# Kernel optimization log

Measured on AMD Instinct MI355X. Metric: run time of the kernel, lower is better.

## Reference

```python
import jax, jax.numpy as jnp
import numpy as np

B, NQ, NK, E, H, F, L = 8, 300, 4096, 256, 8, 2048, 6
D = E // H
SCALE = D ** -0.5


def _ln(x, g, b):
    m = x.mean(-1, keepdims=True)
    v = ((x - m) ** 2).mean(-1, keepdims=True)
    return (x - m) / jnp.sqrt(v + 1e-5) * g + b


def _split_heads(x):
    b, n, _ = x.shape
    return x.reshape(b, n, H, D).transpose(0, 2, 1, 3)  # (B,H,N,D)


def _merge_heads(x):
    b, h, n, d = x.shape
    return x.transpose(0, 2, 1, 3).reshape(b, n, h * d)


def setup_inputs() -> dict:
    key = jax.random.key(0)
    c = [0]
    def nk():
        c[0] += 1
        return jax.random.fold_in(key, c[0])
    def p(shape):
        return jax.random.normal(nk(), shape, jnp.float32) * 0.02
    return {
        "tgt": jax.random.normal(nk(), (B, NQ, E), jnp.float32),
        "memory": jax.random.normal(nk(), (B, NK, E), jnp.float32),
        "geometry_mask": jax.random.randint(nk(), (B, NQ, NK), 0, 2).astype(bool),
        "sa_wqkv": p((L, 3 * E, E)), "sa_bqkv": p((L, 3 * E)),
        "sa_wo": p((L, E, E)), "sa_bo": p((L, E)),
        "ca_wq": p((L, E, E)), "ca_bq": p((L, E)),
        "ca_wk": p((L, E, E)), "ca_bk": p((L, E)),
        "ca_wv": p((L, E, E)), "ca_bv": p((L, E)),
        "ca_wo": p((L, E, E)), "ca_bo": p((L, E)),
        "f_w1": p((L, F, E)), "f_b1": p((L, F)),
        "f_w2": p((L, E, F)), "f_b2": p((L, E)),
        "ln1g": jnp.ones((L, E)), "ln1b": jnp.zeros((L, E)),
        "ln2g": jnp.ones((L, E)), "ln2b": jnp.zeros((L, E)),
        "ln3g": jnp.ones((L, E)), "ln3b": jnp.zeros((L, E)),
        "lnfg": jnp.ones((E,)), "lnfb": jnp.zeros((E,)),
    }


def _forward(tgt, memory, geometry_mask, params):
    mask4 = geometry_mask[:, None, :, :]  # (B,1,NQ,NK), broadcast over heads

    def step(t, p):
        (wqkv, bqkv, wo, bo, wq, bq, wk, bk, wv, bv, wco, bco,
         w1, b1, w2, b2, g1, be1, g2, be2, g3, be3) = p
        # --- self-attention (torch nn.MultiheadAttention, eval mode) ---
        qkv = t @ wqkv.T + bqkv
        q, k, v = jnp.split(qkv, 3, axis=-1)
        q, k, v = _split_heads(q), _split_heads(k), _split_heads(v)
        a = jax.nn.softmax(jnp.einsum('bhqd,bhkd->bhqk', q, k) * SCALE, axis=-1)
        sa = _merge_heads(jnp.einsum('bhqk,bhkd->bhqd', a, v)) @ wo.T + bo
        t = _ln(t + sa, g1, be1)
        # --- geometry-constrained cross-attention ---
        q = _split_heads(t @ wq.T + bq)
        k = _split_heads(memory @ wk.T + bk)
        v = _split_heads(memory @ wv.T + bv)
        s = jnp.einsum('bhqd,bhkd->bhqk', q, k) * SCALE
        s = jnp.where(mask4, s, -jnp.inf)  # masked_fill(~mask, -inf)
        a = jax.nn.softmax(s, axis=-1)
        ca = _merge_heads(jnp.einsum('bhqk,bhkd->bhqd', a, v)) @ wco.T + bco
        t = _ln(t + ca, g2, be2)
        # --- FFN ---
        f = jax.nn.relu(t @ w1.T + b1) @ w2.T + b2
        t = _ln(t + f, g3, be3)
        return t, None

    out, _ = jax.lax.scan(step, tgt, params)
    return out


def reference(tgt, memory, geometry_mask, sa_wqkv, sa_bqkv, sa_wo, sa_bo,
              ca_wq, ca_bq, ca_wk, ca_bk, ca_wv, ca_bv, ca_wo, ca_bo,
              f_w1, f_b1, f_w2, f_b2, ln1g, ln1b, ln2g, ln2b, ln3g, ln3b,
              lnfg, lnfb):
    params = (sa_wqkv, sa_bqkv, sa_wo, sa_bo, ca_wq, ca_bq, ca_wk, ca_bk,
              ca_wv, ca_bv, ca_wo, ca_bo, f_w1, f_b1, f_w2, f_b2,
              ln1g, ln1b, ln2g, ln2b, ln3g, ln3b)
    out = _forward(tgt, memory, geometry_mask, params)
    return _ln(out, lnfg, lnfb)
```

## Files before the change

### kernel.cpp

```cpp
#include <hip/hip_runtime.h>
#include <hip/hip_bf16.h>

constexpr int cB = 8, cNQ = 300, cNK = 4096, cE = 256, cH = 8, cD = 32, cF = 2048, cL = 6;
constexpr int MT = cB * cNQ;
constexpr int MM = cB * cNK;
constexpr int cQT = 10;
constexpr int cKS = 4;
constexpr float kScale = 0.17677669529663687f;

typedef __attribute__((ext_vector_type(8))) short short8_t;
typedef __attribute__((ext_vector_type(4))) short short4_t;
typedef __attribute__((ext_vector_type(4))) float float4_t;

__device__ inline short f2bf(float x) {
  __hip_bfloat16 h = __float2bfloat16(x);
  return __builtin_bit_cast(short, h);
}

__global__ void init_t(const float* __restrict__ in, float* __restrict__ t,
                       __hip_bfloat16* __restrict__ tb, int n) {
  int i = blockIdx.x * 256 + threadIdx.x;
  if (i < n) { float v = in[i]; t[i] = v; tb[i] = __float2bfloat16(v); }
}
__global__ void cast_f32_bf16(const float* __restrict__ in, __hip_bfloat16* __restrict__ out, int n) {
  int i = blockIdx.x * 256 + threadIdx.x;
  if (i < n) out[i] = __float2bfloat16(in[i]);
}

__global__ void pack_mask_T(const int* __restrict__ m, unsigned* __restrict__ mT) {
  int key = blockIdx.x * 256 + threadIdx.x;
  int qt = blockIdx.y, b = blockIdx.z;
  unsigned w = 0;
  for (int j = 0; j < 32; ++j) {
    int q = qt * 32 + j;
    unsigned bit = (q < cNQ) ? (unsigned)(m[((size_t)b * cNQ + q) * cNK + key] != 0) : 0u;
    w |= bit << j;
  }
  mT[((size_t)b * cQT + qt) * cNK + key] = w;
}

template<typename TA, typename TW, int EPI, int OMODE, typename TOUT>
__global__ __launch_bounds__(256) void gemm_mfma(const TA* __restrict__ A,
                                                 const TW* __restrict__ W,
                                                 const float* __restrict__ bias,
                                                 TOUT* __restrict__ C,
                                                 int M, int N, int K) {
  constexpr int LDSS = 72;
  __shared__ short As[64][LDSS];
  __shared__ short Ws[64][LDSS];
  int tid = threadIdx.x;
  int bm = blockIdx.x * 64, bn = blockIdx.y * 64;
  int lane = tid & 63, wave = tid >> 6;
  int m16 = lane & 15, quad = lane >> 4;
  int wm = (wave >> 1) * 32, wn = (wave & 1) * 32;

  int srow = tid >> 2;
  int kc = (tid & 3) * 16;
  bool aok = (bm + srow) < M;

  float4_t acc[2][2];
#pragma unroll
  for (int i = 0; i < 2; ++i)
#pragma unroll
    for (int j = 0; j < 2; ++j) acc[i][j] = (float4_t){0.f, 0.f, 0.f, 0.f};

  for (int k0 = 0; k0 < K; k0 += 64) {
    if constexpr (__hip_internal::is_same<TA, float>::value) {
      const float* src = A + (size_t)(bm + srow) * K + k0 + kc;
      short8_t p0, p1;
#pragma unroll
      for (int u = 0; u < 8; ++u) p0[u] = aok ? f2bf(src[u]) : (short)0;
#pragma unroll
      for (int u = 0; u < 8; ++u) p1[u] = aok ? f2bf(src[8 + u]) : (short)0;
      *(short8_t*)&As[srow][kc] = p0;
      *(short8_t*)&As[srow][kc + 8] = p1;
    } else {
      const TA* src = A + (size_t)(bm + srow) * K + k0 + kc;
      short8_t z = 0;
      *(short8_t*)&As[srow][kc] = aok ? *(const short8_t*)src : z;
      *(short8_t*)&As[srow][kc + 8] = aok ? *(const short8_t*)(src + 8) : z;
    }
    if constexpr (__hip_internal::is_same<TW, float>::value) {
      const float* src = W + (size_t)(bn + srow) * K + k0 + kc;
      short8_t p0, p1;
#pragma unroll
      for (int u = 0; u < 8; ++u) p0[u] = f2bf(src[u]);
#pragma unroll
      for (int u = 0; u < 8; ++u) p1[u] = f2bf(src[8 + u]);
      *(short8_t*)&Ws[srow][kc] = p0;
      *(short8_t*)&Ws[srow][kc + 8] = p1;
    } else {
      const TW* src = W + (size_t)(bn + srow) * K + k0 + kc;
      *(short8_t*)&Ws[srow][kc] = *(const short8_t*)src;
      *(short8_t*)&Ws[srow][kc + 8] = *(const short8_t*)(src + 8);
    }
    __syncthreads();
#pragma unroll
    for (int kk = 0; kk < 2; ++kk) {
      short8_t aF[2], bF[2];
#pragma unroll
      for (int i = 0; i < 2; ++i)
        aF[i] = *(const short8_t*)&As[wm + i * 16 + m16][kk * 32 + quad * 8];
#pragma unroll
      for (int j = 0; j < 2; ++j)
        bF[j] = *(const short8_t*)&Ws[wn + j * 16 + m16][kk * 32 + quad * 8];
#pragma unroll
      for (int i = 0; i < 2; ++i)
#pragma unroll
        for (int j = 0; j < 2; ++j)
          acc[i][j] = __builtin_amdgcn_mfma_f32_16x16x32_bf16(aF[i], bF[j], acc[i][j], 0, 0, 0);
    }
    __syncthreads();
  }

  if constexpr (OMODE == 2) {
#pragma unroll
    for (int i = 0; i < 2; ++i)
#pragma unroll
      for (int r = 0; r < 4; ++r) {
        int ml = wm + i * 16 + quad * 4 + r;
#pragma unroll
        for (int j = 0; j < 2; ++j) {
          int nl = wn + j * 16 + m16;
          Ws[nl][ml] = f2bf(acc[i][j][r] + bias[bn + nl]);
        }
      }
    __syncthreads();
    int nl = tid >> 2, mc = (tid & 3) * 16;
    if (bm + mc < M) {
      int n = bn + nl;
      __hip_bfloat16* dst = (__hip_bfloat16*)C +
          ((size_t)(n >> 5) * 32 + (n & 31)) * (size_t)M + bm + mc;
      *(short8_t*)dst = *(const short8_t*)&Ws[nl][mc];
      *(short8_t*)(dst + 8) = *(const short8_t*)&Ws[nl][mc + 8];
    }
  } else {
#pragma unroll
    for (int i = 0; i < 2; ++i) {
#pragma unroll
      for (int r = 0; r < 4; ++r) {
        int m = bm + wm + i * 16 + quad * 4 + r;
        if (m >= M) continue;
#pragma unroll
        for (int j = 0; j < 2; ++j) {
          int n = bn + wn + j * 16 + m16;
          float v = acc[i][j][r] + bias[n];
          if (EPI == 1) v = fmaxf(v, 0.f);
          if constexpr (OMODE == 1) {
            ((__hip_bfloat16*)C)[((size_t)(n >> 5) * M + m) * 32 + (n & 31)] = __float2bfloat16(v);
          } else if constexpr (__hip_internal::is_same<TOUT, float>::value) {
            C[(size_t)m * N + n] = v;
          } else {
            C[(size_t)m * N + n] = __float2bfloat16(v);
          }
        }
      }
    }
  }
}

template<typename TW, int EPI, int OMODE, typename TOUT>
__global__ __launch_bounds__(256) void gemm128(const __hip_bfloat16* __restrict__ A,
                                               const TW* __restrict__ W,
                                               const float* __restrict__ bias,
                                               TOUT* __restrict__ C,
                                               int M, int N, int K) {
  __shared__ short lds[2 * 128 * 72];
  auto As = (short(*)[72])lds;
  auto Ws = (short(*)[72])(lds + 128 * 72);
  int tid = threadIdx.x;
  int bm = blockIdx.x * 128, bn = blockIdx.y * 128;
  int lane = tid & 63, wave = tid >> 6;
  int n16 = lane & 15, quad = lane >> 4;
  int wm = (wave >> 1) * 64, wn = (wave & 1) * 64;
  int srow = tid >> 1, kc = (tid & 1) * 32;
  bool aok = (bm + srow) < M;

  float4_t acc[4][4];
#pragma unroll
  for (int i = 0; i < 4; ++i)
#pragma unroll
    for (int j = 0; j < 4; ++j) acc[i][j] = (float4_t){0.f, 0.f, 0.f, 0.f};

  for (int k0 = 0; k0 < K; k0 += 64) {
    {
      const __hip_bfloat16* src = A + (size_t)(bm + srow) * K + k0 + kc;
      short8_t z = 0;
#pragma unroll
      for (int u = 0; u < 4; ++u)
        *(short8_t*)&As[srow][kc + u * 8] = aok ? *(const short8_t*)(src + u * 8) : z;
    }
    if constexpr (__hip_internal::is_same<TW, float>::value) {
      const float* src = W + (size_t)(bn + srow) * K + k0 + kc;
#pragma unroll
      for (int u = 0; u < 4; ++u) {
        short8_t p;
#pragma unroll
        for (int v = 0; v < 8; ++v) p[v] = f2bf(src[u * 8 + v]);
        *(short8_t*)&Ws[srow][kc + u * 8] = p;
      }
    } else {
      const TW* src = W + (size_t)(bn + srow) * K + k0 + kc;
#pragma unroll
      for (int u = 0; u < 4; ++u)
        *(short8_t*)&Ws[srow][kc + u * 8] = *(const short8_t*)(src + u * 8);
    }
    __syncthreads();
#pragma unroll
    for (int kk = 0; kk < 2; ++kk) {
      short8_t aF[4], bF[4];
#pragma unroll
      for (int i = 0; i < 4; ++i)
        aF[i] = *(const short8_t*)&As[wm + i * 16 + n16][kk * 32 + quad * 8];
#pragma unroll
      for (int j = 0; j < 4; ++j)
        bF[j] = *(const short8_t*)&Ws[wn + j * 16 + n16][kk * 32 + quad * 8];
#pragma unroll
      for (int i = 0; i < 4; ++i)
#pragma unroll
        for (int j = 0; j < 4; ++j)
          acc[i][j] = __builtin_amdgcn_mfma_f32_16x16x32_bf16(aF[i], bF[j], acc[i][j], 0, 0, 0);
    }
    __syncthreads();
  }

  if constexpr (OMODE == 2) {
    auto TT = (short(*)[128])lds;
#pragma unroll
    for (int i = 0; i < 4; ++i)
#pragma unroll
      for (int r = 0; r < 4; ++r) {
        int ml = wm + i * 16 + quad * 4 + r;
#pragma unroll
        for (int j = 0; j < 4; ++j) {
          int nl = wn + j * 16 + n16;
          TT[nl][ml] = f2bf(acc[i][j][r] + bias[bn + nl]);
        }
      }
    __syncthreads();
    int nl = tid >> 1, mh = (tid & 1) * 64;
    int n = bn + nl;
    __hip_bfloat16* dst = (__hip_bfloat16*)C +
        ((size_t)(n >> 5) * 32 + (n & 31)) * (size_t)M + bm + mh;
#pragma unroll
    for (int ch = 0; ch < 8; ++ch) {
      if (bm + mh + ch * 8 < M)
        *(short8_t*)(dst + ch * 8) = *(const short8_t*)&TT[nl][mh + ch * 8];
    }
  } else {
#pragma unroll
    for (int i = 0; i < 4; ++i) {
#pragma unroll
      for (int r = 0; r < 4; ++r) {
        int m = bm + wm + i * 16 + quad * 4 + r;
        if (m >= M) continue;
#pragma unroll
        for (int j = 0; j < 4; ++j) {
          int n = bn + wn + j * 16 + n16;
          float v = acc[i][j][r] + bias[n];
          if (EPI == 1) v = fmaxf(v, 0.f);
          if constexpr (OMODE == 1) {
            ((__hip_bfloat16*)C)[((size_t)(n >> 5) * M + m) * 32 + (n & 31)] = __float2bfloat16(v);
          } else if constexpr (__hip_internal::is_same<TOUT, float>::value) {
            C[(size_t)m * N + n] = v;
          } else {
            C[(size_t)m * N + n] = __float2bfloat16(v);
          }
        }
      }
    }
  }
}

template<typename TQ, bool MASKED>
__global__ __launch_bounds__(256) void attn_flash(
    const TQ* __restrict__ qb, size_t strQb, size_t strQh, int qRowStr,
    const __hip_bfloat16* __restrict__ kb, size_t strKb, size_t strKh, int kRowStr,
    const __hip_bfloat16* __restrict__ vt, size_t strVb, size_t strVh, size_t strVd,
    const unsigned* __restrict__ mT, size_t strMb,
    float* __restrict__ pO, size_t pStrO,
    float* __restrict__ pL, size_t pStrL,
    int nq, int nk, int kChunk) {
  int hb = blockIdx.x;
  int h = hb & 7, bz = hb >> 3;
  int qt = blockIdx.y, ks = blockIdx.z;
  int qbase = qt * 32;

  const TQ* q = qb + (size_t)bz * strQb + (size_t)h * strQh;
  const __hip_bfloat16* K = kb + (size_t)bz * strKb + (size_t)h * strKh;
  const __hip_bfloat16* V = vt + (size_t)bz * strVb + (size_t)h * strVh;
  const unsigned* mrow = MASKED ? (mT + (size_t)bz * strMb + (size_t)qt * cNK) : nullptr;

  int tid = threadIdx.x;
  int lane = tid & 63, wave = tid >> 6;
  int n16 = lane & 15, quad = lane >> 4;

  __shared__ float redO[4][32][33];
  __shared__ float redL[4][32];
  short* sPw = (short*)&redO[0][0][0] + wave * (32 * 40);

  short8_t qf[2];
#pragma unroll
  for (int qi = 0; qi < 2; ++qi) {
    qf[qi] = 0;
    int qr = qbase + qi * 16 + n16;
    if (qr < nq) {
      const TQ* qp = q + (size_t)qr * qRowStr + quad * 8;
      if constexpr (__hip_internal::is_same<TQ, float>::value) {
#pragma unroll
        for (int j = 0; j < 8; ++j) qf[qi][j] = f2bf(qp[j]);
      } else {
        qf[qi] = *(const short8_t*)qp;
      }
    }
  }
  short8_t ones;
#pragma unroll
  for (int j = 0; j < 8; ++j) ones[j] = f2bf(1.0f);

  float4_t accO[2][2], accL[2];
#pragma unroll
  for (int qi = 0; qi < 2; ++qi) {
    accL[qi] = (float4_t){0.f, 0.f, 0.f, 0.f};
#pragma unroll
    for (int di = 0; di < 2; ++di) accO[qi][di] = (float4_t){0.f, 0.f, 0.f, 0.f};
  }
  float4_t zero4 = {0.f, 0.f, 0.f, 0.f};

  int kpad = (nk + 31) & ~31;
  int kend = ks * kChunk + kChunk;
  if (kend > kpad) kend = kpad;
  for (int koff = ks * kChunk + wave * 32; koff < kend; koff += 128) {
    int k0 = koff + 2 * n16;
    unsigned w0 = 0xFFFFFFFFu, w1 = 0xFFFFFFFFu;
    if (MASKED) {
      const unsigned* mp = mrow + k0;
      w0 = mp[0]; w1 = mp[1];
    }
    bool in0 = k0 < nk, in1 = (k0 + 1) < nk;
    short8_t kf0 = *(const short8_t*)(K + (size_t)k0 * kRowStr + quad * 8);
    short8_t kf1 = *(const short8_t*)(K + (size_t)(k0 + 1) * kRowStr + quad * 8);
    short8_t vf0 = *(const short8_t*)(V + (size_t)n16 * strVd + koff + quad * 8);
    short8_t vf1 = *(const short8_t*)(V + (size_t)(16 + n16) * strVd + koff + quad * 8);
    __builtin_amdgcn_s_setprio(1);
    float4_t s00 = __builtin_amdgcn_mfma_f32_16x16x32_bf16(qf[0], kf0, zero4, 0, 0, 0);
    float4_t s01 = __builtin_amdgcn_mfma_f32_16x16x32_bf16(qf[0], kf1, zero4, 0, 0, 0);
    float4_t s10 = __builtin_amdgcn_mfma_f32_16x16x32_bf16(qf[1], kf0, zero4, 0, 0, 0);
    float4_t s11 = __builtin_amdgcn_mfma_f32_16x16x32_bf16(qf[1], kf1, zero4, 0, 0, 0);
    __builtin_amdgcn_s_setprio(0);
#pragma unroll
    for (int qi = 0; qi < 2; ++qi) {
      const float4_t& sa = qi ? s10 : s00;
      const float4_t& sb = qi ? s11 : s01;
#pragma unroll
      for (int r = 0; r < 4; ++r) {
        int row = qi * 16 + quad * 4 + r;
        bool ok0 = in0, ok1 = in1;
        if (MASKED) {
          ok0 = ok0 && ((w0 >> row) & 1u);
          ok1 = ok1 && ((w1 >> row) & 1u);
        }
        float p0 = ok0 ? __expf(sa[r] * kScale) : 0.f;
        float p1 = ok1 ? __expf(sb[r] * kScale) : 0.f;
        unsigned pw = (unsigned)(unsigned short)f2bf(p0) |
                      ((unsigned)(unsigned short)f2bf(p1) << 16);
        *(unsigned*)&sPw[row * 40 + 2 * n16] = pw;
      }
    }
    __builtin_amdgcn_s_setprio(1);
#pragma unroll
    for (int qi = 0; qi < 2; ++qi) {
      short8_t pf = *(const short8_t*)&sPw[(qi * 16 + n16) * 40 + quad * 8];
      accO[qi][0] = __builtin_amdgcn_mfma_f32_16x16x32_bf16(pf, vf0, accO[qi][0], 0, 0, 0);
      accO[qi][1] = __builtin_amdgcn_mfma_f32_16x16x32_bf16(pf, vf1, accO[qi][1], 0, 0, 0);
      accL[qi]    = __builtin_amdgcn_mfma_f32_16x16x32_bf16(pf, ones, accL[qi], 0, 0, 0);
    }
    __builtin_amdgcn_s_setprio(0);
  }

  __syncthreads();
#pragma unroll
  for (int qi = 0; qi < 2; ++qi) {
#pragma unroll
    for (int r = 0; r < 4; ++r) {
      int row = qi * 16 + quad * 4 + r;
#pragma unroll
      for (int di = 0; di < 2; ++di)
        redO[wave][row][di * 16 + n16] = accO[qi][di][r];
      if (n16 == 0) redL[wave][row] = accL[qi][r];
    }
  }
  __syncthreads();

  size_t oBase = (size_t)ks * pStrO + (size_t)(bz * cNQ) * 256 + h * 32;
  int row = tid >> 3, c0 = (tid & 7) * 4;
  if (qbase + row < nq) {
    float4_t o;
#pragma unroll
    for (int u = 0; u < 4; ++u)
      o[u] = redO[0][row][c0 + u] + redO[1][row][c0 + u] +
             redO[2][row][c0 + u] + redO[3][row][c0 + u];
    *(float4_t*)&pO[oBase + (size_t)(qbase + row) * 256 + c0] = o;
  }
  if (tid < 32 && qbase + tid < nq) {
    float l = redL[0][tid] + redL[1][tid] + redL[2][tid] + redL[3][tid];
    pL[(size_t)ks * pStrL + (size_t)hb * 320 + qbase + tid] = l;
  }
}

__global__ __launch_bounds__(64) void attn_merge(const float* __restrict__ pO,
                                                 const float* __restrict__ pL,
                                                 __hip_bfloat16* __restrict__ out) {
  int row = blockIdx.x;
  int lane = threadIdx.x;
  int c0 = lane * 4;
  int bz = row / cNQ, qq = row - bz * cNQ;
  int h = c0 >> 5;
  float l = 0.f;
#pragma unroll
  for (int ks = 0; ks < cKS; ++ks)
    l += pL[(size_t)ks * (64 * 320) + (size_t)(bz * 8 + h) * 320 + qq];
  float inv = 1.f / l;
  float o[4] = {0.f, 0.f, 0.f, 0.f};
#pragma unroll
  for (int ks = 0; ks < cKS; ++ks) {
    const float4_t v = *(const float4_t*)&pO[(size_t)ks * (MT * 256) + (size_t)row * 256 + c0];
#pragma unroll
    for (int u = 0; u < 4; ++u) o[u] += v[u];
  }
  short4_t res = {f2bf(o[0] * inv), f2bf(o[1] * inv), f2bf(o[2] * inv), f2bf(o[3] * inv)};
  *(short4_t*)&out[(size_t)row * 256 + c0] = res;
}

__global__ __launch_bounds__(64) void add_ln_k(float* __restrict__ t,
                                               __hip_bfloat16* __restrict__ tb,
                                               const float* __restrict__ delta,
                                               const float* __restrict__ g,
                                               const float* __restrict__ bb) {
  int r = blockIdx.x, lane = threadIdx.x;
  size_t base = (size_t)r * cE + lane * 4;
  float x[4];
  float s = 0.f;
#pragma unroll
  for (int i = 0; i < 4; ++i) { x[i] = t[base + i] + delta[base + i]; s += x[i]; }
  for (int off = 32; off; off >>= 1) s += __shfl_xor(s, off);
  float mean = s * (1.f / cE);
  float v = 0.f;
#pragma unroll
  for (int i = 0; i < 4; ++i) { float dd = x[i] - mean; v += dd * dd; }
  for (int off = 32; off; off >>= 1) v += __shfl_xor(v, off);
  float rstd = rsqrtf(v * (1.f / cE) + 1e-5f);
  float y[4];
#pragma unroll
  for (int i = 0; i < 4; ++i) {
    y[i] = (x[i] - mean) * rstd * g[lane * 4 + i] + bb[lane * 4 + i];
    t[base + i] = y[i];
  }
  short4_t pb = {f2bf(y[0]), f2bf(y[1]), f2bf(y[2]), f2bf(y[3])};
  *(short4_t*)&tb[base] = pb;
}

__global__ __launch_bounds__(64) void final_ln_k(const float* __restrict__ t,
                                                 const float* __restrict__ g,
                                                 const float* __restrict__ bb,
                                                 float* __restrict__ out) {
  int r = blockIdx.x, lane = threadIdx.x;
  size_t base = (size_t)r * cE + lane * 4;
  float x[4];
  float s = 0.f;
#pragma unroll
  for (int i = 0; i < 4; ++i) { x[i] = t[base + i]; s += x[i]; }
  for (int off = 32; off; off >>= 1) s += __shfl_xor(s, off);
  float mean = s * (1.f / cE);
  float v = 0.f;
#pragma unroll
  for (int i = 0; i < 4; ++i) { float dd = x[i] - mean; v += dd * dd; }
  for (int off = 32; off; off >>= 1) v += __shfl_xor(v, off);
  float rstd = rsqrtf(v * (1.f / cE) + 1e-5f);
#pragma unroll
  for (int i = 0; i < 4; ++i)
    out[base + i] = (x[i] - mean) * rstd * g[lane * 4 + i] + bb[lane * 4 + i];
}

struct Bufs {
  float *t, *s1, *s2, *pO, *pL;
  __hip_bfloat16 *tb, *big2, *vtq, *s1b, *s2b, *qbf, *ffnh, *kbuf, *vtb, *membf;
  unsigned* mTr;
  const float* memory;
  bool fullKV, precast;
};

template<typename TW>
static void run_layers(const TW* const* wt, const float* const* bs,
                       const float* ln1g, const float* ln1b,
                       const float* ln2g, const float* ln2b,
                       const float* ln3g, const float* ln3b,
                       Bufs B, hipStream_t stream) {
  const size_t pStrO = (size_t)MT * 256, pStrL = 64 * 320;
  for (int l = 0; l < cL; ++l) {
    const TW* wqkv = wt[0] + (size_t)l * 3 * cE * cE;  const float* bqkv = bs[0] + (size_t)l * 3 * cE;
    const TW* wo   = wt[1] + (size_t)l * cE * cE;      const float* bo   = bs[1] + (size_t)l * cE;
    const TW* wq   = wt[2] + (size_t)l * cE * cE;      const float* bq   = bs[2] + (size_t)l * cE;
    const TW* wk   = wt[3] + (size_t)l * cE * cE;      const float* bk   = bs[3] + (size_t)l * cE;
    const TW* wv   = wt[4] + (size_t)l * cE * cE;      const float* bv   = bs[4] + (size_t)l * cE;
    const TW* wco  = wt[5] + (size_t)l * cE * cE;      const float* bco  = bs[5] + (size_t)l * cE;
    const TW* w1   = wt[6] + (size_t)l * cF * cE;      const float* b1   = bs[6] + (size_t)l * cF;
    const TW* w2   = wt[7] + (size_t)l * cE * cF;      const float* b2   = bs[7] + (size_t)l * cE;

    gemm_mfma<__hip_bfloat16, TW, 0, 0, __hip_bfloat16><<<dim3(38, 8), 256, 0, stream>>>(
        B.tb, wqkv, bqkv, B.big2, MT, 512, cE);
    gemm_mfma<__hip_bfloat16, TW, 0, 2, __hip_bfloat16><<<dim3(38, 4), 256, 0, stream>>>(
        B.tb, wqkv + (size_t)512 * cE, bqkv + 512, B.vtq, MT, cE, cE);
    attn_flash<__hip_bfloat16, false><<<dim3(64, cQT, cKS), 256, 0, stream>>>(
        B.big2, (size_t)cNQ * 512, 32, 512,
        B.big2 + 256, (size_t)cNQ * 512, 32, 512,
        B.vtq, 300, (size_t)cD * MT, MT,
        nullptr, 0,
        B.pO, pStrO, B.pL, pStrL, cNQ, cNQ, 96);
    attn_merge<<<MT, 64, 0, stream>>>(B.pO, B.pL, B.s1b);
    gemm_mfma<__hip_bfloat16, TW, 0, 0, float><<<dim3(38, 4), 256, 0, stream>>>(
        B.s1b, wo, bo, B.s2, MT, cE, cE);
    add_ln_k<<<MT, 64, 0, stream>>>(B.t, B.tb, B.s2, ln1g + (size_t)l * cE, ln1b + (size_t)l * cE);
    gemm_mfma<__hip_bfloat16, TW, 0, 0, __hip_bfloat16><<<dim3(38, 4), 256, 0, stream>>>(
        B.tb, wq, bq, B.qbf, MT, cE, cE);
    if (B.fullKV && B.precast) {
      gemm128<TW, 0, 1, __hip_bfloat16><<<dim3(256, 2), 256, 0, stream>>>(
          B.membf, wk, bk, B.kbuf, MM, cE, cE);
      gemm128<TW, 0, 2, __hip_bfloat16><<<dim3(256, 2), 256, 0, stream>>>(
          B.membf, wv, bv, B.vtb, MM, cE, cE);
      attn_flash<__hip_bfloat16, true><<<dim3(64, cQT, cKS), 256, 0, stream>>>(
          B.qbf, (size_t)cNQ * cE, 32, cE,
          B.kbuf, (size_t)cNK * cD, (size_t)MM * cD, cD,
          B.vtb, (size_t)cNK, (size_t)cD * MM, MM,
          B.mTr, (size_t)cQT * cNK,
          B.pO, pStrO, B.pL, pStrL, cNQ, cNK, 1024);
      attn_merge<<<MT, 64, 0, stream>>>(B.pO, B.pL, B.s2b);
    } else {
      for (int b = 0; b < cB; ++b) {
        const float* memb = B.memory + (size_t)b * cNK * cE;
        gemm_mfma<float, TW, 0, 1, __hip_bfloat16><<<dim3(64, 4), 256, 0, stream>>>(
            memb, wk, bk, B.kbuf, cNK, cE, cE);
        gemm_mfma<float, TW, 0, 2, __hip_bfloat16><<<dim3(64, 4), 256, 0, stream>>>(
            memb, wv, bv, B.vtb, cNK, cE, cE);
        attn_flash<__hip_bfloat16, true><<<dim3(8, cQT, cKS), 256, 0, stream>>>(
            B.qbf + (size_t)b * cNQ * cE, 0, 32, cE,
            B.kbuf, 0, (size_t)cNK * cD, cD,
            B.vtb, 0, (size_t)cD * cNK, cNK,
            B.mTr + (size_t)b * cQT * cNK, 0,
            B.pO + (size_t)b * cNQ * 256, pStrO, B.pL + (size_t)b * 8 * 320, pStrL,
            cNQ, cNK, 1024);
      }
      attn_merge<<<MT, 64, 0, stream>>>(B.pO, B.pL, B.s2b);
    }
    gemm_mfma<__hip_bfloat16, TW, 0, 0, float><<<dim3(38, 4), 256, 0, stream>>>(
        B.s2b, wco, bco, B.s1, MT, cE, cE);
    add_ln_k<<<MT, 64, 0, stream>>>(B.t, B.tb, B.s1, ln2g + (size_t)l * cE, ln2b + (size_t)l * cE);
    gemm128<TW, 1, 0, __hip_bfloat16><<<dim3(19, 16), 256, 0, stream>>>(
        B.tb, w1, b1, B.ffnh, MT, cF, cE);
    gemm_mfma<__hip_bfloat16, TW, 0, 0, float><<<dim3(38, 4), 256, 0, stream>>>(
        B.ffnh, w2, b2, B.s1, MT, cE, cF);
    add_ln_k<<<MT, 64, 0, stream>>>(B.t, B.tb, B.s1, ln3g + (size_t)l * cE, ln3b + (size_t)l * cE);
  }
}

extern "C" void kernel_launch(void* const* d_in, const int* in_sizes, int n_in,
                              void* d_out, int out_size, void* d_ws, size_t ws_size,
                              hipStream_t stream) {
  (void)in_sizes; (void)n_in; (void)out_size;
  const float* tgt    = (const float*)d_in[0];
  const float* memory = (const float*)d_in[1];
  const int*   gmask  = (const int*)d_in[2];
  const float* w_in[8]  = {(const float*)d_in[3], (const float*)d_in[5], (const float*)d_in[7],
                           (const float*)d_in[9], (const float*)d_in[11], (const float*)d_in[13],
                           (const float*)d_in[15], (const float*)d_in[17]};
  const float* b_in[8]  = {(const float*)d_in[4], (const float*)d_in[6], (const float*)d_in[8],
                           (const float*)d_in[10], (const float*)d_in[12], (const float*)d_in[14],
                           (const float*)d_in[16], (const float*)d_in[18]};
  const size_t w_sz[8]  = {(size_t)cL*3*cE*cE, (size_t)cL*cE*cE, (size_t)cL*cE*cE,
                           (size_t)cL*cE*cE, (size_t)cL*cE*cE, (size_t)cL*cE*cE,
                           (size_t)cL*cF*cE, (size_t)cL*cE*cF};
  const float* ln1g = (const float*)d_in[19], *ln1b = (const float*)d_in[20];
  const float* ln2g = (const float*)d_in[21], *ln2b = (const float*)d_in[22];
  const float* ln3g = (const float*)d_in[23], *ln3b = (const float*)d_in[24];
  const float* lnfg = (const float*)d_in[25], *lnfb = (const float*)d_in[26];

  char* wp = (char*)d_ws;
  auto alloc = [&](size_t bytes) { void* p = wp; wp += (bytes + 255) & ~(size_t)255; return p; };

  Bufs B;
  B.memory = memory;
  B.t  = (float*)alloc((size_t)MT * cE * 4);
  B.s1 = (float*)alloc((size_t)MT * cE * 4);
  B.s2 = (float*)alloc((size_t)MT * cE * 4);
  B.tb = (__hip_bfloat16*)alloc((size_t)MT * cE * 2);
  B.big2 = (__hip_bfloat16*)alloc((size_t)MT * 512 * 2);
  B.vtq  = (__hip_bfloat16*)alloc((size_t)cH * cD * MT * 2);
  B.mTr = (unsigned*)alloc((size_t)cB * cQT * cNK * 4);
  B.pO = (float*)alloc((size_t)cKS * MT * 256 * 4);
  B.pL = (float*)alloc((size_t)cKS * 64 * 320 * 4);
  B.s1b = B.big2;
  B.s2b = B.big2 + (size_t)MT * 256;
  B.qbf = (__hip_bfloat16*)B.s1;
  B.ffnh = (__hip_bfloat16*)B.pO;

  size_t kvFull = (size_t)cH * MM * cD * 2;
  size_t used = (size_t)(wp - (char*)d_ws);
  B.fullKV = ws_size >= used + 2 * kvFull;
  if (B.fullKV) {
    B.kbuf = (__hip_bfloat16*)alloc(kvFull);
    B.vtb  = (__hip_bfloat16*)alloc(kvFull);
  } else {
    B.kbuf = (__hip_bfloat16*)alloc((size_t)cH * cNK * cD * 2);
    B.vtb  = (__hip_bfloat16*)alloc((size_t)cH * cNK * cD * 2);
  }
  size_t memBytes = (size_t)MM * cE * 2;
  used = (size_t)(wp - (char*)d_ws);
  B.precast = B.fullKV && (ws_size >= used + memBytes);
  B.membf = B.precast ? (__hip_bfloat16*)alloc(memBytes) : nullptr;

  size_t wbfTotal = 0;
  for (int i = 0; i < 8; ++i) wbfTotal += ((w_sz[i] * 2 + 255) & ~(size_t)255);
  used = (size_t)(wp - (char*)d_ws);
  bool wPre = ws_size >= used + wbfTotal;
  __hip_bfloat16* wbf[8] = {};
  if (wPre)
    for (int i = 0; i < 8; ++i) wbf[i] = (__hip_bfloat16*)alloc(w_sz[i] * 2);

  init_t<<<(MT * cE + 255) / 256, 256, 0, stream>>>(tgt, B.t, B.tb, MT * cE);
  pack_mask_T<<<dim3(cNK / 256, cQT, cB), 256, 0, stream>>>(gmask, B.mTr);
  if (B.precast)
    cast_f32_bf16<<<(MM * cE + 255) / 256, 256, 0, stream>>>(memory, B.membf, MM * cE);
  if (wPre)
    for (int i = 0; i < 8; ++i)
      cast_f32_bf16<<<(int)((w_sz[i] + 255) / 256), 256, 0, stream>>>(w_in[i], wbf[i], (int)w_sz[i]);

  if (wPre) {
    const __hip_bfloat16* wt[8];
    for (int i = 0; i < 8; ++i) wt[i] = wbf[i];
    run_layers<__hip_bfloat16>(wt, b_in, ln1g, ln1b, ln2g, ln2b, ln3g, ln3b, B, stream);
  } else {
    run_layers<float>(w_in, b_in, ln1g, ln1b, ln2g, ln2b, ln3g, ln3b, B, stream);
  }

  final_ln_k<<<MT, 64, 0, stream>>>(B.t, lnfg, lnfb, (float*)d_out);
}
```

Baseline: 1.282 ms.

## Add small-tile gemm32 for E-wide GEMMs and fold softmax scale into Q projection

Adds a 32x64-tile MFMA GEMM kernel and uses it for the four N=256 projections (out-proj, cross Q, cross out, FFN down). The smaller tiles launch 300 blocks instead of 152, so more CUs have work. The Q projections are pre-scaled by scale*log2(e), which lets the attention kernels use exp2f directly. Masking now multiplies by a float 0/1 instead of branching, and bf16 packing uses a paired conversion. The small-tile GEMM trades parallelism for less data reuse and no double buffering, notably on the K=2048 FFN GEMM.

```diff
diff --git a/kernel.cpp b/kernel.cpp
--- a/kernel.cpp
+++ b/kernel.cpp
@@ -7,6 +7,7 @@
 constexpr int cQT = 10;
 constexpr int cKS = 4;
 constexpr float kScale = 0.17677669529663687f;
+constexpr float kC2 = 0.25506601f;
 
 typedef __attribute__((ext_vector_type(8))) short short8_t;
 typedef __attribute__((ext_vector_type(4))) short short4_t;
@@ -15,6 +16,13 @@
 __device__ inline short f2bf(float x) {
   __hip_bfloat16 h = __float2bfloat16(x);
   return __builtin_bit_cast(short, h);
+}
+
+__device__ inline unsigned pack_bf16x2(float a, float b) {
+  __hip_bfloat162 pp = __float22bfloat162_rn(make_float2(a, b));
+  unsigned r;
+  __builtin_memcpy(&r, &pp, 4);
+  return r;
 }
 
 __global__ void init_t(const float* __restrict__ in, float* __restrict__ t,
@@ -146,6 +154,8 @@
           int n = bn + wn + j * 16 + m16;
           float v = acc[i][j][r] + bias[n];
           if (EPI == 1) v = fmaxf(v, 0.f);
+          if (EPI == 2 && n < 256) v *= kC2;
+          if (EPI == 3) v *= kC2;
           if constexpr (OMODE == 1) {
             ((__hip_bfloat16*)C)[((size_t)(n >> 5) * M + m) * 32 + (n & 31)] = __float2bfloat16(v);
           } else if constexpr (__hip_internal::is_same<TOUT, float>::value) {
@@ -154,6 +164,82 @@
             C[(size_t)m * N + n] = __float2bfloat16(v);
           }
         }
+      }
+    }
+  }
+}
+
+template<typename TW, int EPI, typename TOUT>
+__global__ __launch_bounds__(256) void gemm32(const __hip_bfloat16* __restrict__ A,
+                                              const TW* __restrict__ W,
+                                              const float* __restrict__ bias,
+                                              TOUT* __restrict__ C,
+                                              int M, int N, int K) {
+  __shared__ short As[32][72];
+  __shared__ short Ws[64][72];
+  int tid = threadIdx.x;
+  int bm = blockIdx.x * 32, bn = blockIdx.y * 64;
+  int lane = tid & 63, wave = tid >> 6;
+  int m16 = lane & 15, quad = lane >> 4;
+  int wn = wave * 16;
+
+  int sa_row = tid >> 3, sa_c = (tid & 7) * 8;
+  int sw_row = tid >> 2, sw_c = (tid & 3) * 16;
+  bool aok = (bm + sa_row) < M;
+
+  float4_t acc[2];
+  acc[0] = (float4_t){0.f, 0.f, 0.f, 0.f};
+  acc[1] = (float4_t){0.f, 0.f, 0.f, 0.f};
+
+  for (int k0 = 0; k0 < K; k0 += 64) {
+    {
+      const __hip_bfloat16* src = A + (size_t)(bm + sa_row) * K + k0 + sa_c;
+      short8_t z = 0;
+      *(short8_t*)&As[sa_row][sa_c] = aok ? *(const short8_t*)src : z;
+    }
+    if constexpr (__hip_internal::is_same<TW, float>::value) {
+      const float* src = W + (size_t)(bn + sw_row) * K + k0 + sw_c;
+      short8_t p0, p1;
+#pragma unroll
+      for (int u = 0; u < 8; ++u) p0[u] = f2bf(src[u]);
+#pragma unroll
+      for (int u = 0; u < 8; ++u) p1[u] = f2bf(src[8 + u]);
+      *(short8_t*)&Ws[sw_row][sw_c] = p0;
+      *(short8_t*)&Ws[sw_row][sw_c + 8] = p1;
+    } else {
+      const TW* src = W + (size_t)(bn + sw_row) * K + k0 + sw_c;
+      *(short8_t*)&Ws[sw_row][sw_c] = *(const short8_t*)src;
+      *(short8_t*)&Ws[sw_row][sw_c + 8] = *(const short8_t*)(src + 8);
+    }
+    __syncthreads();
+#pragma unroll
+    for (int kk = 0; kk < 2; ++kk) {
+      short8_t aF[2], bF;
+#pragma unroll
+      for (int i = 0; i < 2; ++i)
+        aF[i] = *(const short8_t*)&As[i * 16 + m16][kk * 32 + quad * 8];
+      bF = *(const short8_t*)&Ws[wn + m16][kk * 32 + quad * 8];
+#pragma unroll
+      for (int i = 0; i < 2; ++i)
+        acc[i] = __builtin_amdgcn_mfma_f32_16x16x32_bf16(aF[i], bF, acc[i], 0, 0, 0);
+    }
+    __syncthreads();
+  }
+
+#pragma unroll
+  for (int i = 0; i < 2; ++i) {
+#pragma unroll
+    for (int r = 0; r < 4; ++r) {
+      int m = bm + i * 16 + quad * 4 + r;
+      if (m >= M) continue;
+      int n = bn + wn + m16;
+      float v = acc[i][r] + bias[n];
+      if (EPI == 1) v = fmaxf(v, 0.f);
+      if (EPI == 3) v *= kC2;
+      if constexpr (__hip_internal::is_same<TOUT, float>::value) {
+        C[(size_t)m * N + n] = v;
+      } else {
+        C[(size_t)m * N + n] = __float2bfloat16(v);
       }
     }
   }
@@ -332,12 +418,15 @@
   if (kend > kpad) kend = kpad;
   for (int koff = ks * kChunk + wave * 32; koff < kend; koff += 128) {
     int k0 = koff + 2 * n16;
-    unsigned w0 = 0xFFFFFFFFu, w1 = 0xFFFFFFFFu;
+    unsigned w0 = 0, w1 = 0;
+    float okf0 = 1.f, okf1 = 1.f;
     if (MASKED) {
-      const unsigned* mp = mrow + k0;
-      w0 = mp[0]; w1 = mp[1];
-    }
-    bool in0 = k0 < nk, in1 = (k0 + 1) < nk;
+      uint2 mw = *(const uint2*)(mrow + k0);
+      w0 = mw.x; w1 = mw.y;
+    } else {
+      okf0 = (k0 < nk) ? 1.f : 0.f;
+      okf1 = (k0 + 1 < nk) ? 1.f : 0.f;
+    }
     short8_t kf0 = *(const short8_t*)(K + (size_t)k0 * kRowStr + quad * 8);
     short8_t kf1 = *(const short8_t*)(K + (size_t)(k0 + 1) * kRowStr + quad * 8);
     short8_t vf0 = *(const short8_t*)(V + (size_t)n16 * strVd + koff + quad * 8);
@@ -355,16 +444,16 @@
 #pragma unroll
       for (int r = 0; r < 4; ++r) {
         int row = qi * 16 + quad * 4 + r;
-        bool ok0 = in0, ok1 = in1;
+        float m0, m1;
         if (MASKED) {
-          ok0 = ok0 && ((w0 >> row) & 1u);
-          ok1 = ok1 && ((w1 >> row) & 1u);
+          m0 = (float)((w0 >> row) & 1u);
+          m1 = (float)((w1 >> row) & 1u);
+        } else {
+          m0 = okf0; m1 = okf1;
         }
-        float p0 = ok0 ? __expf(sa[r] * kScale) : 0.f;
-        float p1 = ok1 ? __expf(sb[r] * kScale) : 0.f;
-        unsigned pw = (unsigned)(unsigned short)f2bf(p0) |
-                      ((unsigned)(unsigned short)f2bf(p1) << 16);
-        *(unsigned*)&sPw[row * 40 + 2 * n16] = pw;
+        float p0 = exp2f(sa[r]) * m0;
+        float p1 = exp2f(sb[r]) * m1;
+        *(unsigned*)&sPw[row * 40 + 2 * n16] = pack_bf16x2(p0, p1);
       }
     }
     __builtin_amdgcn_s_setprio(1);
@@ -507,7 +596,7 @@
     const TW* w1   = wt[6] + (size_t)l * cF * cE;      const float* b1   = bs[6] + (size_t)l * cF;
     const TW* w2   = wt[7] + (size_t)l * cE * cF;      const float* b2   = bs[7] + (size_t)l * cE;
 
-    gemm_mfma<__hip_bfloat16, TW, 0, 0, __hip_bfloat16><<<dim3(38, 8), 256, 0, stream>>>(
+    gemm_mfma<__hip_bfloat16, TW, 2, 0, __hip_bfloat16><<<dim3(38, 8), 256, 0, stream>>>(
         B.tb, wqkv, bqkv, B.big2, MT, 512, cE);
     gemm_mfma<__hip_bfloat16, TW, 0, 2, __hip_bfloat16><<<dim3(38, 4), 256, 0, stream>>>(
         B.tb, wqkv + (size_t)512 * cE, bqkv + 512, B.vtq, MT, cE, cE);
@@ -518,10 +607,10 @@
         nullptr, 0,
         B.pO, pStrO, B.pL, pStrL, cNQ, cNQ, 96);
     attn_merge<<<MT, 64, 0, stream>>>(B.pO, B.pL, B.s1b);
-    gemm_mfma<__hip_bfloat16, TW, 0, 0, float><<<dim3(38, 4), 256, 0, stream>>>(
+    gemm32<TW, 0, float><<<dim3(75, 4), 256, 0, stream>>>(
         B.s1b, wo, bo, B.s2, MT, cE, cE);
     add_ln_k<<<MT, 64, 0, stream>>>(B.t, B.tb, B.s2, ln1g + (size_t)l * cE, ln1b + (size_t)l * cE);
-    gemm_mfma<__hip_bfloat16, TW, 0, 0, __hip_bfloat16><<<dim3(38, 4), 256, 0, stream>>>(
+    gemm32<TW, 3, __hip_bfloat16><<<dim3(75, 4), 256, 0, stream>>>(
         B.tb, wq, bq, B.qbf, MT, cE, cE);
     if (B.fullKV && B.precast) {
       gemm128<TW, 0, 1, __hip_bfloat16><<<dim3(256, 2), 256, 0, stream>>>(
@@ -552,12 +641,12 @@
       }
       attn_merge<<<MT, 64, 0, stream>>>(B.pO, B.pL, B.s2b);
     }
-    gemm_mfma<__hip_bfloat16, TW, 0, 0, float><<<dim3(38, 4), 256, 0, stream>>>(
+    gemm32<TW, 0, float><<<dim3(75, 4), 256, 0, stream>>>(
         B.s2b, wco, bco, B.s1, MT, cE, cE);
     add_ln_k<<<MT, 64, 0, stream>>>(B.t, B.tb, B.s1, ln2g + (size_t)l * cE, ln2b + (size_t)l * cE);
     gemm128<TW, 1, 0, __hip_bfloat16><<<dim3(19, 16), 256, 0, stream>>>(
         B.tb, w1, b1, B.ffnh, MT, cF, cE);
-    gemm_mfma<__hip_bfloat16, TW, 0, 0, float><<<dim3(38, 4), 256, 0, stream>>>(
+    gemm32<TW, 0, float><<<dim3(75, 4), 256, 0, stream>>>(
         B.ffnh, w2, b2, B.s1, MT, cE, cF);
     add_ln_k<<<MT, 64, 0, stream>>>(B.t, B.tb, B.s1, ln3g + (size_t)l * cE, ln3b + (size_t)l * cE);
   }
```

Measured after the change: 1.268 ms. About the same (-1.1%).
